# Kernel tuning notes

Hardware: AMD Instinct MI355X
Metric: run time of the kernel (lower is better)

## Reference

```python
import jax, jax.numpy as jnp
import numpy as np

B, IN_CHAN, CHAN, H, W = 8, 64, 64, 56, 56


def setup_inputs() -> dict:
    key = jax.random.key(0)
    k1, k2, k3, k4 = jax.random.split(key, 4)
    x = jax.random.normal(k1, (B, IN_CHAN, H, W), dtype=jnp.float32)
    eye23 = jnp.eye(3, dtype=jnp.float32)[:2]  # [2,3] identity affine
    geoParams = eye23[None, None] + 0.1 * jax.random.normal(k2, (CHAN, IN_CHAN, 2, 3), dtype=jnp.float32)
    linComb = jax.random.uniform(k3, (CHAN, IN_CHAN), dtype=jnp.float32)
    boxParams = eye23[None] + 0.1 * jax.random.normal(k4, (CHAN, 2, 3), dtype=jnp.float32)
    return {"x": x, "geoParams": geoParams, "linComb": linComb, "boxParams": boxParams}


def _sample_coords(theta, Hs, Ws):
    # F.affine_grid with align_corners=False: base grid at pixel centers in [-1,1]
    xs = 2.0 * (jnp.arange(Ws, dtype=jnp.float32) + 0.5) / Ws - 1.0  # [W]
    ys = 2.0 * (jnp.arange(Hs, dtype=jnp.float32) + 0.5) / Hs - 1.0  # [H]
    gx = theta[..., 0, 0, None, None] * xs[None, :] + theta[..., 0, 1, None, None] * ys[:, None] + theta[..., 0, 2, None, None]
    gy = theta[..., 1, 0, None, None] * xs[None, :] + theta[..., 1, 1, None, None] * ys[:, None] + theta[..., 1, 2, None, None]
    # grid_sample unnormalize (align_corners=False)
    ix = ((gx + 1.0) * Ws - 1.0) / 2.0
    iy = ((gy + 1.0) * Hs - 1.0) / 2.0
    return ix, iy  # theta.shape[:-2] + (Hs, Ws)


def _corners(ix, iy, Hs, Ws):
    # bilinear corner flat-indices and weights (zero padding via validity mask)
    ix0 = jnp.floor(ix)
    iy0 = jnp.floor(iy)
    out = []
    for dx in (0.0, 1.0):
        for dy in (0.0, 1.0):
            cx = ix0 + dx
            cy = iy0 + dy
            w = (1.0 - jnp.abs(ix - cx)) * (1.0 - jnp.abs(iy - cy))
            valid = (cx >= 0) & (cx <= Ws - 1) & (cy >= 0) & (cy <= Hs - 1)
            idx = jnp.clip(cy, 0, Hs - 1).astype(jnp.int32) * Ws + jnp.clip(cx, 0, Ws - 1).astype(jnp.int32)
            out.append((idx, w * valid.astype(w.dtype)))
    return out


def reference(x, geoParams, linComb, boxParams):
    Bn, IC, Hs, Ws = x.shape
    C = geoParams.shape[0]
    HW = Hs * Ws
    ix, iy = _sample_coords(geoParams, Hs, Ws)  # [C, IC, H, W]
    flat = x.reshape(Bn, IC, HW)
    ic_idx = jnp.arange(IC)[None, :, None]  # broadcast with [C, IC, HW] indices
    out = jnp.zeros((Bn, C, HW), dtype=x.dtype)
    for idx, w in _corners(ix, iy, Hs, Ws):
        idxf = idx.reshape(C, IC, HW)
        wf = w.reshape(C, IC, HW)
        g = flat[:, ic_idx, idxf]  # [B, C, IC, HW] gathered corner values
        out = out + jnp.einsum('bcip,cip,ci->bcp', g, wf, linComb)
    out = out.reshape(Bn, C, Hs, Ws)
    # BoxPool: grid_sample of an all-ones image == sum of valid corner weights
    bix, biy = _sample_coords(boxParams, Hs, Ws)  # [C, H, W]
    box = jnp.zeros((C, Hs, Ws), dtype=x.dtype)
    for _, w in _corners(bix, biy, Hs, Ws):
        box = box + w
    return out * box[None]
```

## Files before the change

### kernel.cpp

```cpp
#include <hip/hip_runtime.h>

#define NB 8
#define ICN 64
#define NC 64
#define H 56
#define W 56
#define HW (H*W)
#define PH 58
#define PW 58
#define PHW (PH*PW)

typedef __attribute__((ext_vector_type(8))) _Float16 half8;

__global__ __launch_bounds__(256) void setup_kernel(
    const float* __restrict__ x, const float* __restrict__ geo,
    const float* __restrict__ lin,
    _Float16* __restrict__ xt, float* __restrict__ prm)
{
    const int bx = blockIdx.x;
    if (bx < 64) {
        const int i = bx * 256 + threadIdx.x;
        const float t00 = geo[i*6+0], t01 = geo[i*6+1], t02 = geo[i*6+2];
        const float t10 = geo[i*6+3], t11 = geo[i*6+4], t12 = geo[i*6+5];
        prm[i*8+0] = t00;
        prm[i*8+1] = t01;
        prm[i*8+2] = -27.5f*(t00+t01) + 28.f*t02 + 27.5f;
        prm[i*8+3] = t10;
        prm[i*8+4] = t11;
        prm[i*8+5] = -27.5f*(t10+t11) + 28.f*t12 + 27.5f;
        prm[i*8+6] = lin[i];
        prm[i*8+7] = 0.f;
    } else {
        const int id = (bx - 64) * 256 + threadIdx.x;
        const int ic  = id / PHW;
        const int rem = id - ic * PHW;
        const int ph  = rem / PW;
        const int pw  = rem - ph * PW;
        half8 v;
        #pragma unroll
        for (int b = 0; b < NB; ++b) v[b] = (_Float16)0.f;
        if (ph >= 1 && ph <= H && pw >= 1 && pw <= W) {
            const int p = (ph - 1) * W + (pw - 1);
            #pragma unroll
            for (int b = 0; b < NB; ++b)
                v[b] = (_Float16)x[(size_t)b * ICN * HW + ic * HW + p];
        }
        *(half8*)(xt + (size_t)id * NB) = v;
    }
}

__global__ __launch_bounds__(256) void geom_h4_kernel(
    const _Float16* __restrict__ xt,
    const float* __restrict__ prm,
    const float* __restrict__ boxp,
    float* __restrict__ out)
{
    const int c = blockIdx.x;
    const int p = blockIdx.y * 256 + threadIdx.x;
    if (p >= HW) return;
    const int h = p / W;
    const int w = p - h * W;
    const float wf = (float)w, hf = (float)h;

    float acc[NB];
    #pragma unroll
    for (int b = 0; b < NB; ++b) acc[b] = 0.f;

    const float* pp = prm + (size_t)c * ICN * 8;

    for (int icc = 0; icc < ICN; icc += 4) {
        half8 hacc;
        #pragma unroll
        for (int b = 0; b < NB; ++b) hacc[b] = (_Float16)0.f;

        #pragma unroll
        for (int k = 0; k < 4; ++k) {
            const float* q = pp + (icc + k) * 8;
            const float ixf = fmaf(q[0], wf, fmaf(q[1], hf, q[2]));
            const float iyf = fmaf(q[3], wf, fmaf(q[4], hf, q[5]));
            const float l   = q[6];

            const float fcx0 = fminf(fmaxf(floorf(ixf), -1.f), 55.f);
            const float fcy0 = fminf(fmaxf(floorf(iyf), -1.f), 55.f);
            const float wx0 = fmaxf(0.f, 1.f - fabsf(ixf - fcx0));
            const float wx1 = fmaxf(0.f, 1.f - fabsf(ixf - fcx0 - 1.f));
            const float wy0 = fmaxf(0.f, 1.f - fabsf(iyf - fcy0));
            const float wy1 = fmaxf(0.f, 1.f - fabsf(iyf - fcy0 - 1.f));
            const float wy0l = wy0 * l, wy1l = wy1 * l;

            const _Float16 hw00 = (_Float16)(wx0 * wy0l);
            const _Float16 hw10 = (_Float16)(wx1 * wy0l);
            const _Float16 hw01 = (_Float16)(wx0 * wy1l);
            const _Float16 hw11 = (_Float16)(wx1 * wy1l);

            const int i00 = ((int)fcy0) * PW + (int)fcx0 + (PW + 1);
            const _Float16* base = xt + ((size_t)(icc + k) * PHW + i00) * NB;

            const half8 v00 = *(const half8*)(base);
            const half8 v10 = *(const half8*)(base + NB);
            const half8 v01 = *(const half8*)(base + PW * NB);
            const half8 v11 = *(const half8*)(base + (PW + 1) * NB);

            hacc += v00 * hw00 + v10 * hw10 + v01 * hw01 + v11 * hw11;
        }

        #pragma unroll
        for (int b = 0; b < NB; ++b) acc[b] += (float)hacc[b];
    }

    float box;
    {
        const float* bp = boxp + c*6;
        const float xs = 2.0f * (wf + 0.5f) / (float)W - 1.0f;
        const float ys = 2.0f * (hf + 0.5f) / (float)H - 1.0f;
        const float gx = bp[0]*xs + bp[1]*ys + bp[2];
        const float gy = bp[3]*xs + bp[4]*ys + bp[5];
        const float ixf = ((gx + 1.f)*(float)W - 1.f) * 0.5f;
        const float iyf = ((gy + 1.f)*(float)H - 1.f) * 0.5f;
        const float ix0 = floorf(ixf), iy0 = floorf(iyf);
        const float fx = ixf - ix0, fy = iyf - iy0;
        const int cx0 = (int)ix0, cy0 = (int)iy0;
        const int cx1 = cx0 + 1,  cy1 = cy0 + 1;
        const bool vx0 = (cx0 >= 0) && (cx0 < W);
        const bool vx1 = (cx1 >= 0) && (cx1 < W);
        const bool vy0 = (cy0 >= 0) && (cy0 < H);
        const bool vy1 = (cy1 >= 0) && (cy1 < H);
        box = (1.f-fx)*(1.f-fy)*((vx0 && vy0) ? 1.f : 0.f)
            + (1.f-fx)*fy     *((vx0 && vy1) ? 1.f : 0.f)
            + fx*(1.f-fy)     *((vx1 && vy0) ? 1.f : 0.f)
            + fx*fy           *((vx1 && vy1) ? 1.f : 0.f);
    }

    #pragma unroll
    for (int b = 0; b < NB; ++b)
        out[((size_t)b*NC + c)*HW + p] = acc[b] * box;
}

__global__ __launch_bounds__(256) void geom_kernel(
    const float* __restrict__ x, const float* __restrict__ geo,
    const float* __restrict__ lin, const float* __restrict__ boxp,
    float* __restrict__ out)
{
    const int c = blockIdx.x;
    const int p = blockIdx.y * blockDim.x + threadIdx.x;
    if (p >= HW) return;
    const int h = p / W;
    const int w = p - h * W;
    const float xs = 2.0f * ((float)w + 0.5f) / (float)W - 1.0f;
    const float ys = 2.0f * ((float)h + 0.5f) / (float)H - 1.0f;

    float acc[NB];
    #pragma unroll
    for (int b = 0; b < NB; ++b) acc[b] = 0.f;

    const float* gp = geo + c * ICN * 6;
    const float* lc = lin + c * ICN;

    for (int ic = 0; ic < ICN; ++ic) {
        const float t00 = gp[ic*6+0], t01 = gp[ic*6+1], t02 = gp[ic*6+2];
        const float t10 = gp[ic*6+3], t11 = gp[ic*6+4], t12 = gp[ic*6+5];
        const float l = lc[ic];
        const float gx = t00*xs + t01*ys + t02;
        const float gy = t10*xs + t11*ys + t12;
        const float ixf = ((gx + 1.f)*(float)W - 1.f) * 0.5f;
        const float iyf = ((gy + 1.f)*(float)H - 1.f) * 0.5f;
        const float ix0 = floorf(ixf), iy0 = floorf(iyf);
        const float fx = ixf - ix0, fy = iyf - iy0;
        const int cx0 = (int)ix0, cy0 = (int)iy0;
        const int cx1 = cx0 + 1,  cy1 = cy0 + 1;
        const bool vx0 = (cx0 >= 0) && (cx0 <= W-1);
        const bool vx1 = (cx1 >= 0) && (cx1 <= W-1);
        const bool vy0 = (cy0 >= 0) && (cy0 <= H-1);
        const bool vy1 = (cy1 >= 0) && (cy1 <= H-1);
        const float wx0 = 1.f - fx, wx1 = fx;
        const float wy0 = 1.f - fy, wy1 = fy;
        const float w00 = wx0*wy0 * ((vx0 && vy0) ? l : 0.f);
        const float w01 = wx0*wy1 * ((vx0 && vy1) ? l : 0.f);
        const float w10 = wx1*wy0 * ((vx1 && vy0) ? l : 0.f);
        const float w11 = wx1*wy1 * ((vx1 && vy1) ? l : 0.f);
        const int icx0 = min(max(cx0, 0), W-1);
        const int icx1 = min(max(cx1, 0), W-1);
        const int icy0 = min(max(cy0, 0), H-1);
        const int icy1 = min(max(cy1, 0), H-1);
        const int i00 = icy0*W + icx0;
        const int i01 = icy1*W + icx0;
        const int i10 = icy0*W + icx1;
        const int i11 = icy1*W + icx1;
        const float* xp = x + ic * HW;
        #pragma unroll
        for (int b = 0; b < NB; ++b) {
            const float* xb = xp + (size_t)b * ICN * HW;
            acc[b] += w00*xb[i00] + w01*xb[i01] + w10*xb[i10] + w11*xb[i11];
        }
    }

    float box;
    {
        const float* bp = boxp + c*6;
        const float gx = bp[0]*xs + bp[1]*ys + bp[2];
        const float gy = bp[3]*xs + bp[4]*ys + bp[5];
        const float ixf = ((gx + 1.f)*(float)W - 1.f) * 0.5f;
        const float iyf = ((gy + 1.f)*(float)H - 1.f) * 0.5f;
        const float ix0 = floorf(ixf), iy0 = floorf(iyf);
        const float fx = ixf - ix0, fy = iyf - iy0;
        const int cx0 = (int)ix0, cy0 = (int)iy0;
        const int cx1 = cx0 + 1,  cy1 = cy0 + 1;
        const bool vx0 = (cx0 >= 0) && (cx0 < W);
        const bool vx1 = (cx1 >= 0) && (cx1 < W);
        const bool vy0 = (cy0 >= 0) && (cy0 < H);
        const bool vy1 = (cy1 >= 0) && (cy1 < H);
        box = (1.f-fx)*(1.f-fy)*((vx0 && vy0) ? 1.f : 0.f)
            + (1.f-fx)*fy     *((vx0 && vy1) ? 1.f : 0.f)
            + fx*(1.f-fy)     *((vx1 && vy0) ? 1.f : 0.f)
            + fx*fy           *((vx1 && vy1) ? 1.f : 0.f);
    }
    #pragma unroll
    for (int b = 0; b < NB; ++b)
        out[((size_t)b*NC + c)*HW + p] = acc[b] * box;
}

extern "C" void kernel_launch(void* const* d_in, const int* in_sizes, int n_in,
                              void* d_out, int out_size, void* d_ws, size_t ws_size,
                              hipStream_t stream) {
    const float* x    = (const float*)d_in[0];
    const float* geo  = (const float*)d_in[1];
    const float* lin  = (const float*)d_in[2];
    const float* boxp = (const float*)d_in[3];
    float* out = (float*)d_out;

    const size_t xt_bytes  = (size_t)ICN * PHW * NB * sizeof(_Float16);
    const size_t prm_off   = (xt_bytes + 255) & ~(size_t)255;
    const size_t prm_bytes = (size_t)NC * ICN * 8 * sizeof(float);
    if (ws_size >= prm_off + prm_bytes) {
        _Float16* xt = (_Float16*)d_ws;
        float* prm = (float*)((char*)d_ws + prm_off);
        hipLaunchKernelGGL(setup_kernel, dim3(64 + (ICN*PHW)/256), dim3(256),
                           0, stream, x, geo, lin, xt, prm);
        hipLaunchKernelGGL(geom_h4_kernel, dim3(NC, (HW + 255)/256), dim3(256),
                           0, stream, xt, prm, boxp, out);
    } else {
        hipLaunchKernelGGL(geom_kernel, dim3(NC, (HW + 255)/256), dim3(256),
                           0, stream, x, geo, lin, boxp, out);
    }
}
```

Measured before the change: 48.09 us.

## Compute two vertically adjacent pixels per thread, reusing shared bilinear corner loads

Each thread now produces outputs for rows 2h and 2h+1. The second row's sample coordinates come from the first row's plus the y-derivative terms. When the second row's corner cell is exactly one row below the first, it reuses the two bottom corner vectors already loaded and fetches only two new ones, otherwise it does a full four-corner gather. This cuts gather loads and parameter reads per output and halves thread count with 128-thread blocks, at the cost of more registers, a data-dependent branch, and fewer resident waves.

Measured after the change: 58.95 us. 1.23x slower.

```diff
diff --git a/kernel.cpp b/kernel.cpp
--- a/kernel.cpp
+++ b/kernel.cpp
@@ -49,91 +49,119 @@
     }
 }
 
-__global__ __launch_bounds__(256) void geom_h4_kernel(
+__device__ __forceinline__ float box_factor(const float* bp, float wf, float hf) {
+    const float xs = 2.0f * (wf + 0.5f) / (float)W - 1.0f;
+    const float ys = 2.0f * (hf + 0.5f) / (float)H - 1.0f;
+    const float gx = bp[0]*xs + bp[1]*ys + bp[2];
+    const float gy = bp[3]*xs + bp[4]*ys + bp[5];
+    const float ixf = ((gx + 1.f)*(float)W - 1.f) * 0.5f;
+    const float iyf = ((gy + 1.f)*(float)H - 1.f) * 0.5f;
+    const float ix0 = floorf(ixf), iy0 = floorf(iyf);
+    const float fx = ixf - ix0, fy = iyf - iy0;
+    const int cx0 = (int)ix0, cy0 = (int)iy0;
+    const int cx1 = cx0 + 1,  cy1 = cy0 + 1;
+    const bool vx0 = (cx0 >= 0) && (cx0 < W);
+    const bool vx1 = (cx1 >= 0) && (cx1 < W);
+    const bool vy0 = (cy0 >= 0) && (cy0 < H);
+    const bool vy1 = (cy1 >= 0) && (cy1 < H);
+    return (1.f-fx)*(1.f-fy)*((vx0 && vy0) ? 1.f : 0.f)
+         + (1.f-fx)*fy     *((vx0 && vy1) ? 1.f : 0.f)
+         + fx*(1.f-fy)     *((vx1 && vy0) ? 1.f : 0.f)
+         + fx*fy           *((vx1 && vy1) ? 1.f : 0.f);
+}
+
+__global__ __launch_bounds__(128) void geom_p_kernel(
     const _Float16* __restrict__ xt,
     const float* __restrict__ prm,
     const float* __restrict__ boxp,
     float* __restrict__ out)
 {
-    const int c = blockIdx.x;
-    const int p = blockIdx.y * 256 + threadIdx.x;
-    if (p >= HW) return;
-    const int h = p / W;
-    const int w = p - h * W;
-    const float wf = (float)w, hf = (float)h;
-
-    float acc[NB];
-    #pragma unroll
-    for (int b = 0; b < NB; ++b) acc[b] = 0.f;
+    const int c   = blockIdx.x;
+    const int idx = blockIdx.y * 128 + threadIdx.x;
+    const int h2  = idx / W;
+    const int w   = idx - h2 * W;
+    if (h2 >= H/2) return;
+    const float wf = (float)w, hf = (float)(2*h2);
+
+    float accT[NB], accB[NB];
+    #pragma unroll
+    for (int b = 0; b < NB; ++b) { accT[b] = 0.f; accB[b] = 0.f; }
 
     const float* pp = prm + (size_t)c * ICN * 8;
 
     for (int icc = 0; icc < ICN; icc += 4) {
-        half8 hacc;
-        #pragma unroll
-        for (int b = 0; b < NB; ++b) hacc[b] = (_Float16)0.f;
+        half8 haccT, haccB;
+        #pragma unroll
+        for (int b = 0; b < NB; ++b) { haccT[b] = (_Float16)0.f; haccB[b] = (_Float16)0.f; }
 
         #pragma unroll
         for (int k = 0; k < 4; ++k) {
             const float* q = pp + (icc + k) * 8;
-            const float ixf = fmaf(q[0], wf, fmaf(q[1], hf, q[2]));
-            const float iyf = fmaf(q[3], wf, fmaf(q[4], hf, q[5]));
+            const float Bx = q[1], By = q[4];
+            const float ixf = fmaf(q[0], wf, fmaf(Bx, hf, q[2]));
+            const float iyf = fmaf(q[3], wf, fmaf(By, hf, q[5]));
             const float l   = q[6];
-
-            const float fcx0 = fminf(fmaxf(floorf(ixf), -1.f), 55.f);
-            const float fcy0 = fminf(fmaxf(floorf(iyf), -1.f), 55.f);
+            const float ixf2 = ixf + Bx;
+            const float iyf2 = iyf + By;
+
+            const float fcx0 = fminf(fmaxf(floorf(ixf),  -1.f), 55.f);
+            const float fcy0 = fminf(fmaxf(floorf(iyf),  -1.f), 55.f);
+            const float fcx2 = fminf(fmaxf(floorf(ixf2), -1.f), 55.f);
+            const float fcy2 = fminf(fmaxf(floorf(iyf2), -1.f), 55.f);
+
             const float wx0 = fmaxf(0.f, 1.f - fabsf(ixf - fcx0));
             const float wx1 = fmaxf(0.f, 1.f - fabsf(ixf - fcx0 - 1.f));
-            const float wy0 = fmaxf(0.f, 1.f - fabsf(iyf - fcy0));
-            const float wy1 = fmaxf(0.f, 1.f - fabsf(iyf - fcy0 - 1.f));
-            const float wy0l = wy0 * l, wy1l = wy1 * l;
-
-            const _Float16 hw00 = (_Float16)(wx0 * wy0l);
-            const _Float16 hw10 = (_Float16)(wx1 * wy0l);
-            const _Float16 hw01 = (_Float16)(wx0 * wy1l);
-            const _Float16 hw11 = (_Float16)(wx1 * wy1l);
-
-            const int i00 = ((int)fcy0) * PW + (int)fcx0 + (PW + 1);
-            const _Float16* base = xt + ((size_t)(icc + k) * PHW + i00) * NB;
+            const float wy0 = fmaxf(0.f, 1.f - fabsf(iyf - fcy0)) * l;
+            const float wy1 = fmaxf(0.f, 1.f - fabsf(iyf - fcy0 - 1.f)) * l;
+            const _Float16 hw00 = (_Float16)(wx0*wy0), hw10 = (_Float16)(wx1*wy0);
+            const _Float16 hw01 = (_Float16)(wx0*wy1), hw11 = (_Float16)(wx1*wy1);
+
+            const float bx0 = fmaxf(0.f, 1.f - fabsf(ixf2 - fcx2));
+            const float bx1 = fmaxf(0.f, 1.f - fabsf(ixf2 - fcx2 - 1.f));
+            const float by0 = fmaxf(0.f, 1.f - fabsf(iyf2 - fcy2)) * l;
+            const float by1 = fmaxf(0.f, 1.f - fabsf(iyf2 - fcy2 - 1.f)) * l;
+            const _Float16 hb00 = (_Float16)(bx0*by0), hb10 = (_Float16)(bx1*by0);
+            const _Float16 hb01 = (_Float16)(bx0*by1), hb11 = (_Float16)(bx1*by1);
+
+            const int ix0 = (int)fcx0, iy0 = (int)fcy0;
+            const _Float16* base =
+                xt + ((size_t)(icc + k) * PHW + (iy0 + 1) * PW + ix0 + 1) * NB;
 
             const half8 v00 = *(const half8*)(base);
             const half8 v10 = *(const half8*)(base + NB);
             const half8 v01 = *(const half8*)(base + PW * NB);
             const half8 v11 = *(const half8*)(base + (PW + 1) * NB);
-
-            hacc += v00 * hw00 + v10 * hw10 + v01 * hw01 + v11 * hw11;
+            haccT += v00 * hw00 + v10 * hw10 + v01 * hw01 + v11 * hw11;
+
+            half8 a00 = v01, a10 = v11, a01, a11;
+            const bool common = (fcx2 == fcx0) && (fcy2 == fcy0 + 1.f);
+            if (common) {
+                a01 = *(const half8*)(base + 2 * PW * NB);
+                a11 = *(const half8*)(base + (2 * PW + 1) * NB);
+            } else {
+                const _Float16* b2 =
+                    xt + ((size_t)(icc + k) * PHW + ((int)fcy2 + 1) * PW + (int)fcx2 + 1) * NB;
+                a00 = *(const half8*)(b2);
+                a10 = *(const half8*)(b2 + NB);
+                a01 = *(const half8*)(b2 + PW * NB);
+                a11 = *(const half8*)(b2 + (PW + 1) * NB);
+            }
+            haccB += a00 * hb00 + a10 * hb10 + a01 * hb01 + a11 * hb11;
         }
 
         #pragma unroll
-        for (int b = 0; b < NB; ++b) acc[b] += (float)hacc[b];
-    }
-
-    float box;
-    {
-        const float* bp = boxp + c*6;
-        const float xs = 2.0f * (wf + 0.5f) / (float)W - 1.0f;
-        const float ys = 2.0f * (hf + 0.5f) / (float)H - 1.0f;
-        const float gx = bp[0]*xs + bp[1]*ys + bp[2];
-        const float gy = bp[3]*xs + bp[4]*ys + bp[5];
-        const float ixf = ((gx + 1.f)*(float)W - 1.f) * 0.5f;
-        const float iyf = ((gy + 1.f)*(float)H - 1.f) * 0.5f;
-        const float ix0 = floorf(ixf), iy0 = floorf(iyf);
-        const float fx = ixf - ix0, fy = iyf - iy0;
-        const int cx0 = (int)ix0, cy0 = (int)iy0;
-        const int cx1 = cx0 + 1,  cy1 = cy0 + 1;
-        const bool vx0 = (cx0 >= 0) && (cx0 < W);
-        const bool vx1 = (cx1 >= 0) && (cx1 < W);
-        const bool vy0 = (cy0 >= 0) && (cy0 < H);
-        const bool vy1 = (cy1 >= 0) && (cy1 < H);
-        box = (1.f-fx)*(1.f-fy)*((vx0 && vy0) ? 1.f : 0.f)
-            + (1.f-fx)*fy     *((vx0 && vy1) ? 1.f : 0.f)
-            + fx*(1.f-fy)     *((vx1 && vy0) ? 1.f : 0.f)
-            + fx*fy           *((vx1 && vy1) ? 1.f : 0.f);
-    }
-
-    #pragma unroll
-    for (int b = 0; b < NB; ++b)
-        out[((size_t)b*NC + c)*HW + p] = acc[b] * box;
+        for (int b = 0; b < NB; ++b) { accT[b] += (float)haccT[b]; accB[b] += (float)haccB[b]; }
+    }
+
+    const float boxT = box_factor(boxp + c*6, wf, hf);
+    const float boxB = box_factor(boxp + c*6, wf, hf + 1.f);
+
+    const int p = (2*h2) * W + w;
+    #pragma unroll
+    for (int b = 0; b < NB; ++b) {
+        out[((size_t)b*NC + c)*HW + p]     = accT[b] * boxT;
+        out[((size_t)b*NC + c)*HW + p + W] = accB[b] * boxB;
+    }
 }
 
 __global__ __launch_bounds__(256) void geom_kernel(
@@ -194,26 +222,7 @@
         }
     }
 
-    float box;
-    {
-        const float* bp = boxp + c*6;
-        const float gx = bp[0]*xs + bp[1]*ys + bp[2];
-        const float gy = bp[3]*xs + bp[4]*ys + bp[5];
-        const float ixf = ((gx + 1.f)*(float)W - 1.f) * 0.5f;
-        const float iyf = ((gy + 1.f)*(float)H - 1.f) * 0.5f;
-        const float ix0 = floorf(ixf), iy0 = floorf(iyf);
-        const float fx = ixf - ix0, fy = iyf - iy0;
-        const int cx0 = (int)ix0, cy0 = (int)iy0;
-        const int cx1 = cx0 + 1,  cy1 = cy0 + 1;
-        const bool vx0 = (cx0 >= 0) && (cx0 < W);
-        const bool vx1 = (cx1 >= 0) && (cx1 < W);
-        const bool vy0 = (cy0 >= 0) && (cy0 < H);
-        const bool vy1 = (cy1 >= 0) && (cy1 < H);
-        box = (1.f-fx)*(1.f-fy)*((vx0 && vy0) ? 1.f : 0.f)
-            + (1.f-fx)*fy     *((vx0 && vy1) ? 1.f : 0.f)
-            + fx*(1.f-fy)     *((vx1 && vy0) ? 1.f : 0.f)
-            + fx*fy           *((vx1 && vy1) ? 1.f : 0.f);
-    }
+    float box = box_factor(boxp + c*6, (float)w, (float)h);
     #pragma unroll
     for (int b = 0; b < NB; ++b)
         out[((size_t)b*NC + c)*HW + p] = acc[b] * box;
@@ -236,7 +245,7 @@
         float* prm = (float*)((char*)d_ws + prm_off);
         hipLaunchKernelGGL(setup_kernel, dim3(64 + (ICN*PHW)/256), dim3(256),
                            0, stream, x, geo, lin, xt, prm);
-        hipLaunchKernelGGL(geom_h4_kernel, dim3(NC, (HW + 255)/256), dim3(256),
+        hipLaunchKernelGGL(geom_p_kernel, dim3(NC, 13), dim3(128),
                            0, stream, xt, prm, boxp, out);
     } else {
         hipLaunchKernelGGL(geom_kernel, dim3(NC, (HW + 255)/256), dim3(256),
```
